# Kernel optimization log

Hardware: AMD Instinct MI355X
Metric: run time of the kernel (lower is better)

Reference implementation:

```python
import jax, jax.numpy as jnp
import numpy as np

B, S, F = 2, 2048, 1024
H, D = 16, 64
INIT = 0.02


def setup_inputs() -> dict:
    key = jax.random.key(0)
    k1, k2, k3 = jax.random.split(key, 3)
    x = jax.random.normal(k1, (B, S, F), dtype=jnp.float32)
    w_attn = jax.random.normal(k2, (F, 3 * F), dtype=jnp.float32) * INIT
    b_attn = jnp.zeros((3 * F,), dtype=jnp.float32)
    w_proj = jax.random.normal(k3, (F, F), dtype=jnp.float32) * INIT
    b_proj = jnp.zeros((F,), dtype=jnp.float32)
    return {"x": x, "w_attn": w_attn, "b_attn": b_attn, "w_proj": w_proj, "b_proj": b_proj}


def reference(x, w_attn, b_attn, w_proj, b_proj):
    # c_attn: [..., S, F] -> [..., S, 3F]
    qkv = jnp.einsum('bsf,fe->bse', x, w_attn) + b_attn
    q, k, v = jnp.split(qkv, 3, axis=-1)
    # split heads: [..., S, F] -> [..., S, H, D]
    q = q.reshape(q.shape[:-1] + (H, D))
    k = k.reshape(k.shape[:-1] + (H, D))
    v = v.reshape(v.shape[:-1] + (H, D))
    q = q / jnp.sqrt(jnp.asarray(D, dtype=q.dtype))
    # scores: [..., H, Sq, Sk]
    scores = jnp.einsum('bqhd,bkhd->bhqk', q, k)
    seq = x.shape[-2]
    causal = jnp.tril(jnp.ones((seq, seq), dtype=bool))  # [Sq, Sk]
    big_neg = jnp.finfo(scores.dtype).min
    scores = jnp.where(causal, scores, big_neg)
    weights = jax.nn.softmax(scores, axis=-1)
    z = jnp.einsum('bhqk,bkhd->bqhd', weights, v)
    merged = z.reshape(z.shape[:-2] + (F,))
    out = jnp.einsum('bsf,fe->bse', merged, w_proj) + b_proj
    return out
```

## Files before the change

kernel.cpp:

```cpp
#include <hip/hip_runtime.h>

#define B_ 2
#define S_ 2048
#define F_ 1024
#define H_ 16
#define D_ 64

typedef __bf16 bf16x8 __attribute__((ext_vector_type(8)));
typedef float f32x4 __attribute__((ext_vector_type(4)));
typedef float f32x16 __attribute__((ext_vector_type(16)));

union U8 { unsigned int u[4]; bf16x8 v; };

__device__ __forceinline__ unsigned short f2bf(float f) {
    union { float f; unsigned int u; } v;
    v.f = f;
    unsigned int r = v.u + 0x7fffu + ((v.u >> 16) & 1u);
    return (unsigned short)(r >> 16);
}

__device__ __forceinline__ unsigned int cvtpk_bf16(float lo, float hi) {
    unsigned int r;
    asm("v_cvt_pk_bf16_f32 %0, %1, %2" : "=v"(r) : "v"(lo), "v"(hi));
    return r;
}

__device__ __forceinline__ float xhalf_max(float x) {
    return fmaxf(x, __shfl_xor(x, 32));
}
__device__ __forceinline__ float xhalf_sum(float x) {
    return x + __shfl_xor(x, 32);
}

__device__ __forceinline__ void gload16(const unsigned short* g, unsigned short* l) {
    __builtin_amdgcn_global_load_lds(
        (const __attribute__((address_space(1))) unsigned int*)g,
        (__attribute__((address_space(3))) unsigned int*)l,
        16, 0, 0);
}

__global__ void cvt_kernel(const float* __restrict__ in, unsigned short* __restrict__ out, int n4) {
    int i = blockIdx.x * blockDim.x + threadIdx.x;
    if (i >= n4) return;
    float4 v = reinterpret_cast<const float4*>(in)[i];
    ushort4 o;
    o.x = f2bf(v.x); o.y = f2bf(v.y); o.z = f2bf(v.z); o.w = f2bf(v.w);
    reinterpret_cast<ushort4*>(out)[i] = o;
}

__global__ void tcvt_kernel(const float* __restrict__ in, unsigned short* __restrict__ out, int R, int C) {
    __shared__ float t[32][33];
    int r0 = blockIdx.y << 5, c0 = blockIdx.x << 5;
    int tx = threadIdx.x, ty = threadIdx.y;
#pragma unroll
    for (int kk = 0; kk < 4; ++kk)
        t[ty + 8 * kk][tx] = in[(size_t)(r0 + ty + 8 * kk) * C + c0 + tx];
    __syncthreads();
#pragma unroll
    for (int kk = 0; kk < 4; ++kk)
        out[(size_t)(c0 + ty + 8 * kk) * R + r0 + tx] = f2bf(t[tx][ty + 8 * kk]);
}

__global__ __launch_bounds__(256) void gemm_qkv(const unsigned short* __restrict__ A,
                                                const unsigned short* __restrict__ Bt,
                                                const float* __restrict__ bias,
                                                unsigned short* __restrict__ qo,
                                                unsigned short* __restrict__ ko,
                                                unsigned short* __restrict__ vo) {
    __shared__ __align__(16) unsigned short As[2 * 128 * 32];
    __shared__ __align__(16) unsigned short Bs[2 * 128 * 32];
    const int K = 1024, NT = 32;
    int m0 = blockIdx.y << 7, n0 = blockIdx.x << 7;
    int tid = threadIdx.x;
    int w = tid >> 6, l = tid & 63, lg = l >> 4, lr = l & 15;
    int wm = (w >> 1) << 6, wn = (w & 1) << 6;
    f32x4 acc[4][4] = {};

    int sr = tid >> 2, sc = (tid & 3) << 3;
    const unsigned short* Ab = A + (size_t)(m0 + sr) * K + sc;
    const unsigned short* Bb = Bt + (size_t)(n0 + sr) * K + sc;
    const size_t half = (size_t)64 * K;

    gload16(Ab, &As[tid * 8]);
    gload16(Ab + half, &As[2048 + tid * 8]);
    gload16(Bb, &Bs[tid * 8]);
    gload16(Bb + half, &Bs[2048 + tid * 8]);
    __syncthreads();

    for (int t = 0; t < NT; ++t) {
        int cur = (t & 1) * 4096;
        if (t + 1 < NT) {
            int nxt = ((t + 1) & 1) * 4096;
            int ko2 = (t + 1) * 32;
            gload16(Ab + ko2, &As[nxt + tid * 8]);
            gload16(Ab + ko2 + half, &As[nxt + 2048 + tid * 8]);
            gload16(Bb + ko2, &Bs[nxt + tid * 8]);
            gload16(Bb + ko2 + half, &Bs[nxt + 2048 + tid * 8]);
        }
        bf16x8 af[4], bfr[4];
#pragma unroll
        for (int mi = 0; mi < 4; ++mi)
            af[mi] = *reinterpret_cast<const bf16x8*>(&As[cur + (wm + mi * 16 + lr) * 32 + (lg << 3)]);
#pragma unroll
        for (int ni = 0; ni < 4; ++ni)
            bfr[ni] = *reinterpret_cast<const bf16x8*>(&Bs[cur + (wn + ni * 16 + lr) * 32 + (lg << 3)]);
#pragma unroll
        for (int mi = 0; mi < 4; ++mi)
#pragma unroll
            for (int ni = 0; ni < 4; ++ni)
                acc[mi][ni] = __builtin_amdgcn_mfma_f32_16x16x32_bf16(af[mi], bfr[ni], acc[mi][ni], 0, 0, 0);
        __syncthreads();
    }
#pragma unroll
    for (int mi = 0; mi < 4; ++mi) {
#pragma unroll
        for (int ni = 0; ni < 4; ++ni) {
            int col = n0 + wn + ni * 16 + lr;
            float bv = bias[col];
            int part = col >> 10, cc = col & 1023, h = cc >> 6, d = cc & 63;
            int row0 = m0 + wm + mi * 16 + (lg << 2);
            int bb = row0 >> 11, s0 = row0 & 2047;
            int bh = bb * H_ + h;
            if (part == 2) {
                int jt = s0 >> 5, db = d >> 5, kf2 = (s0 >> 4) & 1, hi2 = (s0 >> 3) & 1;
                int ll = (d & 31) | (hi2 << 5), e0 = s0 & 7;
                ushort4 pk;
                unsigned short* p = reinterpret_cast<unsigned short*>(&pk);
#pragma unroll
                for (int r = 0; r < 4; ++r) p[r] = f2bf(acc[mi][ni][r] + bv);
                *reinterpret_cast<ushort4*>(
                    &vo[(size_t)((((bh * 64 + jt) * 2 + db) * 2 + kf2)) * 512 + ll * 8 + e0]) = pk;
            } else {
                unsigned short* dst = part == 0 ? qo : ko;
                float scale = part == 0 ? 0.125f * 1.44269504f : 1.0f;
                int t2 = s0 >> 5, kf2 = d >> 4, e = d & 7;
                int lbase = ((d >> 3) & 1) << 5;
                size_t fb = (size_t)((bh * 64 + t2) * 4 + kf2) * 512 + e;
#pragma unroll
                for (int r = 0; r < 4; ++r) {
                    float vv = (acc[mi][ni][r] + bv) * scale;
                    dst[fb + (size_t)((((s0 + r) & 31) | lbase)) * 8] = f2bf(vv);
                }
            }
        }
    }
}

__global__ __launch_bounds__(256) void gemm_proj(const unsigned short* __restrict__ A,
                                                 const unsigned short* __restrict__ Bt,
                                                 const float* __restrict__ bias,
                                                 float* __restrict__ out) {
    __shared__ __align__(16) unsigned short As[2 * 128 * 32];
    __shared__ __align__(16) unsigned short Bs[2 * 128 * 32];
    const int K = 1024, NT = 32;
    int m0 = blockIdx.y << 7, n0 = blockIdx.x << 7;
    int tid = threadIdx.x;
    int w = tid >> 6, l = tid & 63, lg = l >> 4, lr = l & 15;
    int wm = (w >> 1) << 6, wn = (w & 1) << 6;
    f32x4 acc[4][4] = {};

    int sr = tid >> 2, sc = (tid & 3) << 3;
    const unsigned short* Ab = A + (size_t)(m0 + sr) * K + sc;
    const unsigned short* Bb = Bt + (size_t)(n0 + sr) * K + sc;
    const size_t half = (size_t)64 * K;

    gload16(Ab, &As[tid * 8]);
    gload16(Ab + half, &As[2048 + tid * 8]);
    gload16(Bb, &Bs[tid * 8]);
    gload16(Bb + half, &Bs[2048 + tid * 8]);
    __syncthreads();

    for (int t = 0; t < NT; ++t) {
        int cur = (t & 1) * 4096;
        if (t + 1 < NT) {
            int nxt = ((t + 1) & 1) * 4096;
            int ko2 = (t + 1) * 32;
            gload16(Ab + ko2, &As[nxt + tid * 8]);
            gload16(Ab + ko2 + half, &As[nxt + 2048 + tid * 8]);
            gload16(Bb + ko2, &Bs[nxt + tid * 8]);
            gload16(Bb + ko2 + half, &Bs[nxt + 2048 + tid * 8]);
        }
        bf16x8 af[4], bfr[4];
#pragma unroll
        for (int mi = 0; mi < 4; ++mi)
            af[mi] = *reinterpret_cast<const bf16x8*>(&As[cur + (wm + mi * 16 + lr) * 32 + (lg << 3)]);
#pragma unroll
        for (int ni = 0; ni < 4; ++ni)
            bfr[ni] = *reinterpret_cast<const bf16x8*>(&Bs[cur + (wn + ni * 16 + lr) * 32 + (lg << 3)]);
#pragma unroll
        for (int mi = 0; mi < 4; ++mi)
#pragma unroll
            for (int ni = 0; ni < 4; ++ni)
                acc[mi][ni] = __builtin_amdgcn_mfma_f32_16x16x32_bf16(af[mi], bfr[ni], acc[mi][ni], 0, 0, 0);
        __syncthreads();
    }
#pragma unroll
    for (int mi = 0; mi < 4; ++mi) {
#pragma unroll
        for (int ni = 0; ni < 4; ++ni) {
            int col = n0 + wn + ni * 16 + lr;
            float bv = bias[col];
#pragma unroll
            for (int r = 0; r < 4; ++r) {
                int row = m0 + wm + mi * 16 + (lg << 2) + r;
                out[(size_t)row * F_ + col] = acc[mi][ni][r] + bv;
            }
        }
    }
}

__device__ __forceinline__ void attn_tile32(
    const unsigned short* __restrict__ k, const unsigned short* __restrict__ v,
    int bh, int jt, bool pref, bool diag, int qcol, int hi, size_t lofs,
    const bf16x8 (&qf)[4], bf16x8 (&kcur)[4], bf16x8 (&knxt)[4],
    float &m, float &lsum, f32x16 &ot0, f32x16 &ot1)
{
    bf16x8 vf[4];
    const unsigned short* vp = v + (size_t)(bh * 64 + jt) * 2048 + lofs;
#pragma unroll
    for (int i = 0; i < 4; ++i)
        vf[i] = *reinterpret_cast<const bf16x8*>(vp + i * 512);
    if (pref) {
        const unsigned short* kp = k + (size_t)(bh * 64 + jt + 1) * 2048 + lofs;
#pragma unroll
        for (int kf = 0; kf < 4; ++kf)
            knxt[kf] = *reinterpret_cast<const bf16x8*>(kp + kf * 512);
    }

    f32x16 st = {};
#pragma unroll
    for (int kf = 0; kf < 4; ++kf)
        st = __builtin_amdgcn_mfma_f32_32x32x16_bf16(kcur[kf], qf[kf], st, 0, 0, 0);

    if (diag) {
        int qmh = qcol - 4 * hi;
#pragma unroll
        for (int r = 0; r < 16; ++r) {
            const int kbase = (r & 3) + 8 * (r >> 2);
            st[r] = (kbase > qmh) ? -1e30f : st[r];
        }
    }

    float pm = st[0];
#pragma unroll
    for (int r = 1; r < 16; ++r) pm = fmaxf(pm, st[r]);
    pm = xhalf_max(pm);

    if (!__all(pm <= m + 8.0f)) {
        float mn = fmaxf(m, pm);
        float scl = exp2f(m - mn);
        m = mn;
        lsum *= scl;
        ot0 *= scl;
        ot1 *= scl;
    }

    float ps = 0.f;
#pragma unroll
    for (int r = 0; r < 16; ++r) { st[r] = exp2f(st[r] - m); ps += st[r]; }
    lsum += ps;

    U8 pa0, pa1;
#pragma unroll
    for (int f = 0; f < 2; ++f) {
        unsigned int a0 = cvtpk_bf16(st[f * 8 + 0], st[f * 8 + 1]);
        unsigned int b0 = cvtpk_bf16(st[f * 8 + 4], st[f * 8 + 5]);
        asm("v_permlane32_swap_b32 %0, %1" : "+v"(a0), "+v"(b0));
        unsigned int a1 = cvtpk_bf16(st[f * 8 + 2], st[f * 8 + 3]);
        unsigned int b1 = cvtpk_bf16(st[f * 8 + 6], st[f * 8 + 7]);
        asm("v_permlane32_swap_b32 %0, %1" : "+v"(a1), "+v"(b1));
        U8& pa = f ? pa1 : pa0;
        pa.u[0] = a0; pa.u[1] = a1; pa.u[2] = b0; pa.u[3] = b1;
    }

    ot0 = __builtin_amdgcn_mfma_f32_32x32x16_bf16(vf[0], pa0.v, ot0, 0, 0, 0);
    ot0 = __builtin_amdgcn_mfma_f32_32x32x16_bf16(vf[1], pa1.v, ot0, 0, 0, 0);
    ot1 = __builtin_amdgcn_mfma_f32_32x32x16_bf16(vf[2], pa0.v, ot1, 0, 0, 0);
    ot1 = __builtin_amdgcn_mfma_f32_32x32x16_bf16(vf[3], pa1.v, ot1, 0, 0, 0);
}

__global__ __launch_bounds__(256, 3) void attn_kernel(const unsigned short* __restrict__ q,
                                                      const unsigned short* __restrict__ k,
                                                      const unsigned short* __restrict__ v,
                                                      unsigned short* __restrict__ z) {
    __shared__ __align__(16) float mbuf[3][64][36];
    int bh = blockIdx.x;
    int qt = gridDim.y - 1 - blockIdx.y;
    int q0 = qt << 5;
    int tid = threadIdx.x, w = tid >> 6, l = tid & 63;
    int qcol = l & 31, hi = l >> 5;
    size_t lofs = (size_t)l * 8;

    bf16x8 qf[4];
    {
        const unsigned short* qp = q + (size_t)(bh * 64 + qt) * 2048 + lofs;
#pragma unroll
        for (int kf = 0; kf < 4; ++kf)
            qf[kf] = *reinterpret_cast<const bf16x8*>(qp + kf * 512);
    }

    f32x16 ot0 = {}, ot1 = {};
    float m = -1e30f, lsum = 0.f;

    int ntk = qt + 1;
    int bs = ntk >> 2, rem = ntk & 3;
    int cnt = bs + ((w >= 4 - rem) ? 1 : 0);
    int start = bs * w + ((w - (4 - rem)) > 0 ? (w - (4 - rem)) : 0);
    int end = start + cnt;

    if (cnt > 0) {
        bf16x8 kA[4], kB[4];
        const unsigned short* kp = k + (size_t)(bh * 64 + start) * 2048 + lofs;
#pragma unroll
        for (int kf = 0; kf < 4; ++kf)
            kA[kf] = *reinterpret_cast<const bf16x8*>(kp + kf * 512);

        int jt = start;
        for (;;) {
            attn_tile32(k, v, bh, jt, jt + 1 < end, jt == qt, qcol, hi, lofs,
                        qf, kA, kB, m, lsum, ot0, ot1);
            if (++jt >= end) break;
            attn_tile32(k, v, bh, jt, jt + 1 < end, jt == qt, qcol, hi, lofs,
                        qf, kB, kA, m, lsum, ot0, ot1);
            if (++jt >= end) break;
        }
    }

    lsum = xhalf_sum(lsum);

    if (w) {
        float* row = mbuf[w - 1][l];
        row[0] = m;
        row[1] = lsum;
        *reinterpret_cast<f32x16*>(&row[4]) = ot0;
        *reinterpret_cast<f32x16*>(&row[20]) = ot1;
    }
    __syncthreads();
    if (w == 0) {
        float mw0 = mbuf[0][l][0], mw1 = mbuf[1][l][0], mw2 = mbuf[2][l][0];
        float mm = fmaxf(fmaxf(m, mw0), fmaxf(mw1, mw2));
        float s0 = exp2f(m - mm);
        lsum *= s0; ot0 *= s0; ot1 *= s0;
#pragma unroll
        for (int i = 0; i < 3; ++i) {
            float sw = exp2f(mbuf[i][l][0] - mm);
            lsum += mbuf[i][l][1] * sw;
            f32x16 t0 = *reinterpret_cast<const f32x16*>(&mbuf[i][l][4]);
            f32x16 t1 = *reinterpret_cast<const f32x16*>(&mbuf[i][l][20]);
            ot0 += t0 * sw;
            ot1 += t1 * sw;
        }

        float inv = 1.0f / lsum;
        int b = bh >> 4, h = bh & 15;
        size_t zrow = ((size_t)(b * S_ + q0 + qcol)) * F_ + h * D_;
#pragma unroll
        for (int db = 0; db < 2; ++db) {
#pragma unroll
            for (int rq = 0; rq < 4; ++rq) {
                ushort4 pk;
                unsigned short* pp = reinterpret_cast<unsigned short*>(&pk);
#pragma unroll
                for (int i = 0; i < 4; ++i) {
                    float val = (db == 0 ? ot0[rq * 4 + i] : ot1[rq * 4 + i]) * inv;
                    pp[i] = f2bf(val);
                }
                *reinterpret_cast<ushort4*>(&z[zrow + db * 32 + rq * 8 + hi * 4]) = pk;
            }
        }
    }
}

extern "C" void kernel_launch(void* const* d_in, const int* in_sizes, int n_in,
                              void* d_out, int out_size, void* d_ws, size_t ws_size,
                              hipStream_t stream) {
    const float* x      = (const float*)d_in[0];
    const float* w_attn = (const float*)d_in[1];
    const float* b_attn = (const float*)d_in[2];
    const float* w_proj = (const float*)d_in[3];
    const float* b_proj = (const float*)d_in[4];
    float* out = (float*)d_out;
    char* ws = (char*)d_ws;

    unsigned short* xb   = (unsigned short*)(ws);
    unsigned short* wa_t = (unsigned short*)(ws + 8388608);
    unsigned short* wp_t = (unsigned short*)(ws + 14680064);
    unsigned short* qb   = (unsigned short*)(ws + 16777216);
    unsigned short* kb   = (unsigned short*)(ws + 25165824);
    unsigned short* vb   = (unsigned short*)(ws + 33554432);
    unsigned short* zb   = xb;

    cvt_kernel<<<4096, 256, 0, stream>>>(x, xb, (4096 * 1024) / 4);
    tcvt_kernel<<<dim3(96, 32), dim3(32, 8), 0, stream>>>(w_attn, wa_t, 1024, 3072);
    tcvt_kernel<<<dim3(32, 32), dim3(32, 8), 0, stream>>>(w_proj, wp_t, 1024, 1024);
    gemm_qkv<<<dim3(24, 32), 256, 0, stream>>>(xb, wa_t, b_attn, qb, kb, vb);
    attn_kernel<<<dim3(32, 64), 256, 0, stream>>>(qb, kb, vb, zb);
    gemm_proj<<<dim3(8, 32), 256, 0, stream>>>(zb, wp_t, b_proj, out);
}
```

Baseline: 121.3 us.

## Retile QKV GEMM to 256x256 blocks with swizzled LDS and block remap

Rewrites the QKV projection GEMM to use 256x256 output tiles with 512 threads, a K-step of 64, and an XOR-swizzled LDS layout. A remapped 1D grid is meant to improve L2 reuse. The larger tiles raise data reuse per block and the swizzle is meant to avoid LDS bank conflicts. In exchange, only 192 blocks launch, which is fewer than the CU count, and the kernel uses 128KB of LDS per block.

```diff
diff --git a/kernel.cpp b/kernel.cpp
--- a/kernel.cpp
+++ b/kernel.cpp
@@ -61,64 +61,98 @@
         out[(size_t)(c0 + ty + 8 * kk) * R + r0 + tx] = f2bf(t[tx][ty + 8 * kk]);
 }
 
-__global__ __launch_bounds__(256) void gemm_qkv(const unsigned short* __restrict__ A,
-                                                const unsigned short* __restrict__ Bt,
-                                                const float* __restrict__ bias,
-                                                unsigned short* __restrict__ qo,
-                                                unsigned short* __restrict__ ko,
-                                                unsigned short* __restrict__ vo) {
-    __shared__ __align__(16) unsigned short As[2 * 128 * 32];
-    __shared__ __align__(16) unsigned short Bs[2 * 128 * 32];
-    const int K = 1024, NT = 32;
-    int m0 = blockIdx.y << 7, n0 = blockIdx.x << 7;
+__global__ __launch_bounds__(512, 2) void gemm_qkv(const unsigned short* __restrict__ A,
+                                                   const unsigned short* __restrict__ Bt,
+                                                   const float* __restrict__ bias,
+                                                   unsigned short* __restrict__ qo,
+                                                   unsigned short* __restrict__ ko,
+                                                   unsigned short* __restrict__ vo) {
+    __shared__ __align__(16) unsigned short lds[65536];
+    const int K = 1024;
+    int bid = blockIdx.x;
+    int swz = (bid & 7) * 24 + (bid >> 3);
+    int by = swz / 12, bx = swz % 12;
+    int m0 = by << 8, n0 = bx << 8;
     int tid = threadIdx.x;
-    int w = tid >> 6, l = tid & 63, lg = l >> 4, lr = l & 15;
-    int wm = (w >> 1) << 6, wn = (w & 1) << 6;
-    f32x4 acc[4][4] = {};
-
-    int sr = tid >> 2, sc = (tid & 3) << 3;
-    const unsigned short* Ab = A + (size_t)(m0 + sr) * K + sc;
-    const unsigned short* Bb = Bt + (size_t)(n0 + sr) * K + sc;
-    const size_t half = (size_t)64 * K;
-
-    gload16(Ab, &As[tid * 8]);
-    gload16(Ab + half, &As[2048 + tid * 8]);
-    gload16(Bb, &Bs[tid * 8]);
-    gload16(Bb + half, &Bs[2048 + tid * 8]);
+    int wid = tid >> 6, l = tid & 63, lg = l >> 4, lr = l & 15;
+    int wr = wid >> 2, wc = wid & 3;
+    f32x4 acc[8][4] = {};
+
+    int g0 = tid, g1 = tid + 512;
+    int r0 = g0 >> 3, p0 = g0 & 7;
+    int r1 = g1 >> 3, p1 = g1 & 7;
+    int c0 = (p0 ^ (r0 & 7)) << 3;
+    int c1 = (p1 ^ (r1 & 7)) << 3;
+
+    int xr = (lr & 7) << 3;
+    int csw0 = (lg * 8) ^ xr;
+    int csw1 = (32 + lg * 8) ^ xr;
+
+    const unsigned short* A0 = A + (size_t)(m0 + r0) * K + c0;
+    const unsigned short* A1 = A + (size_t)(m0 + r1) * K + c1;
+    const unsigned short* A2 = A + (size_t)(m0 + 128 + r0) * K + c0;
+    const unsigned short* A3 = A + (size_t)(m0 + 128 + r1) * K + c1;
+    const unsigned short* B0 = Bt + (size_t)(n0 + r0) * K + c0;
+    const unsigned short* B1 = Bt + (size_t)(n0 + r1) * K + c1;
+    const unsigned short* B2 = Bt + (size_t)(n0 + 128 + r0) * K + c0;
+    const unsigned short* B3 = Bt + (size_t)(n0 + 128 + r1) * K + c1;
+
+    {
+        gload16(A0, &lds[g0 * 8]);
+        gload16(A1, &lds[g1 * 8]);
+        gload16(A2, &lds[8192 + g0 * 8]);
+        gload16(A3, &lds[8192 + g1 * 8]);
+        gload16(B0, &lds[16384 + g0 * 8]);
+        gload16(B1, &lds[16384 + g1 * 8]);
+        gload16(B2, &lds[24576 + g0 * 8]);
+        gload16(B3, &lds[24576 + g1 * 8]);
+    }
     __syncthreads();
 
-    for (int t = 0; t < NT; ++t) {
-        int cur = (t & 1) * 4096;
-        if (t + 1 < NT) {
-            int nxt = ((t + 1) & 1) * 4096;
-            int ko2 = (t + 1) * 32;
-            gload16(Ab + ko2, &As[nxt + tid * 8]);
-            gload16(Ab + ko2 + half, &As[nxt + 2048 + tid * 8]);
-            gload16(Bb + ko2, &Bs[nxt + tid * 8]);
-            gload16(Bb + ko2 + half, &Bs[nxt + 2048 + tid * 8]);
-        }
-        bf16x8 af[4], bfr[4];
-#pragma unroll
-        for (int mi = 0; mi < 4; ++mi)
-            af[mi] = *reinterpret_cast<const bf16x8*>(&As[cur + (wm + mi * 16 + lr) * 32 + (lg << 3)]);
-#pragma unroll
-        for (int ni = 0; ni < 4; ++ni)
-            bfr[ni] = *reinterpret_cast<const bf16x8*>(&Bs[cur + (wn + ni * 16 + lr) * 32 + (lg << 3)]);
-#pragma unroll
-        for (int mi = 0; mi < 4; ++mi)
-#pragma unroll
-            for (int ni = 0; ni < 4; ++ni)
-                acc[mi][ni] = __builtin_amdgcn_mfma_f32_16x16x32_bf16(af[mi], bfr[ni], acc[mi][ni], 0, 0, 0);
+    for (int t = 0; t < 16; ++t) {
+        int bo = (t & 1) * 32768;
+        if (t < 15) {
+            int no = ((t + 1) & 1) * 32768;
+            int t64 = (t + 1) * 64;
+            gload16(A0 + t64, &lds[no + g0 * 8]);
+            gload16(A1 + t64, &lds[no + g1 * 8]);
+            gload16(A2 + t64, &lds[no + 8192 + g0 * 8]);
+            gload16(A3 + t64, &lds[no + 8192 + g1 * 8]);
+            gload16(B0 + t64, &lds[no + 16384 + g0 * 8]);
+            gload16(B1 + t64, &lds[no + 16384 + g1 * 8]);
+            gload16(B2 + t64, &lds[no + 24576 + g0 * 8]);
+            gload16(B3 + t64, &lds[no + 24576 + g1 * 8]);
+        }
+        bf16x8 Bf[8];
+#pragma unroll
+        for (int ni = 0; ni < 4; ++ni) {
+            int rowB = wc * 64 + ni * 16 + lr;
+            int ba = bo + 16384 + (rowB >> 7) * 8192 + (rowB & 127) * 64;
+            Bf[ni * 2]     = *reinterpret_cast<const bf16x8*>(&lds[ba + csw0]);
+            Bf[ni * 2 + 1] = *reinterpret_cast<const bf16x8*>(&lds[ba + csw1]);
+        }
+#pragma unroll
+        for (int mi = 0; mi < 8; ++mi) {
+            int aa = bo + wr * 8192 + (mi * 16 + lr) * 64;
+            bf16x8 a0 = *reinterpret_cast<const bf16x8*>(&lds[aa + csw0]);
+            bf16x8 a1 = *reinterpret_cast<const bf16x8*>(&lds[aa + csw1]);
+#pragma unroll
+            for (int ni = 0; ni < 4; ++ni) {
+                acc[mi][ni] = __builtin_amdgcn_mfma_f32_16x16x32_bf16(a0, Bf[ni * 2], acc[mi][ni], 0, 0, 0);
+                acc[mi][ni] = __builtin_amdgcn_mfma_f32_16x16x32_bf16(a1, Bf[ni * 2 + 1], acc[mi][ni], 0, 0, 0);
+            }
+        }
         __syncthreads();
     }
-#pragma unroll
-    for (int mi = 0; mi < 4; ++mi) {
+
+#pragma unroll
+    for (int mi = 0; mi < 8; ++mi) {
 #pragma unroll
         for (int ni = 0; ni < 4; ++ni) {
-            int col = n0 + wn + ni * 16 + lr;
+            int col = n0 + wc * 64 + ni * 16 + lr;
             float bv = bias[col];
             int part = col >> 10, cc = col & 1023, h = cc >> 6, d = cc & 63;
-            int row0 = m0 + wm + mi * 16 + (lg << 2);
+            int row0 = m0 + wr * 128 + mi * 16 + (lg << 2);
             int bb = row0 >> 11, s0 = row0 & 2047;
             int bh = bb * H_ + h;
             if (part == 2) {
@@ -393,7 +427,7 @@
     cvt_kernel<<<4096, 256, 0, stream>>>(x, xb, (4096 * 1024) / 4);
     tcvt_kernel<<<dim3(96, 32), dim3(32, 8), 0, stream>>>(w_attn, wa_t, 1024, 3072);
     tcvt_kernel<<<dim3(32, 32), dim3(32, 8), 0, stream>>>(w_proj, wp_t, 1024, 1024);
-    gemm_qkv<<<dim3(24, 32), 256, 0, stream>>>(xb, wa_t, b_attn, qb, kb, vb);
+    gemm_qkv<<<192, 512, 0, stream>>>(xb, wa_t, b_attn, qb, kb, vb);
     attn_kernel<<<dim3(32, 64), 256, 0, stream>>>(qb, kb, vb, zb);
     gemm_proj<<<dim3(8, 32), 256, 0, stream>>>(zb, wp_t, b_proj, out);
 }
```

Result: faster. 114.7 us (-5.4%).
